# Kernel tuning notes

Hardware: AMD Instinct MI355X
Metric: run time of the kernel (lower is better)

## Reference

```python
import jax, jax.numpy as jnp
import numpy as np

# Dims: L list entries, T hutch samples, D = output_dim*inducing_size, H = 16 hidden
L, T, D, H = 32, 64, 8192, 16


def setup_inputs() -> dict:
    key = jax.random.key(0)
    k = jax.random.split(key, 4)
    return {
        "u": jax.random.normal(k[0], (L, D), jnp.float32),
        "w": jax.random.normal(k[1], (L, T, D), jnp.float32),  # Hutchinson Gaussian probes
        "W1": jax.random.normal(k[2], (H, D), jnp.float32) / np.sqrt(D).astype(np.float32),
        "b1": jnp.zeros((H,), jnp.float32),
        "W2": jax.random.normal(k[3], (D, H), jnp.float32) / np.sqrt(H).astype(np.float32),
        "b2": jnp.zeros((D,), jnp.float32),
    }


def reference(u, w, W1, b1, W2, b2):
    # f = W2 tanh(W1 u + b1) + b2 ; Jacobian J = W2 diag(1 - h^2) W1
    h = jnp.tanh(u @ W1.T + b1)                 # [L, H]
    f = h @ W2.T + b2                           # [L, D]  (f_u_list stacked)
    s = 1.0 - h * h                             # tanh' at preactivation, [L, H]
    # u_grad = J^T w  computed without materializing J: W1^T diag(s) W2^T w
    v = jnp.einsum('ltd,dh->lth', w, W2)        # W2^T w, [L, T, H]
    v = v * s[:, None, :]                       # diag(s) applied
    g = jnp.einsum('lth,hd->ltd', v, W1)        # J^T w, [L, T, D]
    traces = jnp.sum(g * w, axis=-1)            # w^T J w, [L, T]
    # mean over hutch samples, then mean over list entries -> [1, 1] like torch.mm output
    trace_final_mean = jnp.mean(traces).reshape(1, 1)
    return f, trace_final_mean
```

## Files before the change

### kernel.cpp

```cpp
#include <hip/hip_runtime.h>

typedef __attribute__((ext_vector_type(8))) short bf16x8;
typedef __attribute__((ext_vector_type(4))) float f32x4;

namespace {
constexpr int L = 32, T = 64, D = 8192, H = 16;
constexpr int M = L * T;
constexpr int KP = 32;
constexpr int CHUNK = D / KP;

constexpr size_t WS_WH  = 0;
constexpr size_t WS_WL  = WS_WH + 32 * 8192 / 2;
constexpr size_t WS_PRE = WS_WL + 32 * 8192 / 2;
constexpr size_t WS_AC  = WS_PRE + 32 * 8 * 16;
}

__device__ inline void split1(float f, short& h, short& l) {
  unsigned b = __float_as_uint(f);
  h = (short)(b >> 16);
  float lf = f - __uint_as_float(b & 0xFFFF0000u);
  l = (short)(__float_as_uint(lf) >> 16);
}

__device__ inline void split8(float4 a0, float4 a1, bf16x8& h, bf16x8& l) {
  float f[8] = {a0.x, a0.y, a0.z, a0.w, a1.x, a1.y, a1.z, a1.w};
#pragma unroll
  for (int i = 0; i < 8; ++i) {
    short hh, ll;
    split1(f[i], hh, ll);
    h[i] = hh; l[i] = ll;
  }
}

__global__ __launch_bounds__(256) void k_setup(
    const float* __restrict__ u, const float* __restrict__ W1,
    const float* __restrict__ W2,
    ushort* __restrict__ wh, ushort* __restrict__ wl,
    float* __restrict__ pre, float* __restrict__ ac,
    float* __restrict__ out) {
  int b = blockIdx.x, tid = threadIdx.x;
  if (b == 0 && tid == 0) out[(size_t)L * D] = 0.f;
  if (b < 32) {
    int d = b * 256 + tid;
    const float4* src = reinterpret_cast<const float4*>(W2 + (size_t)d * 16);
    float4 q0 = src[0], q1 = src[1], q2 = src[2], q3 = src[3];
    float v[16] = {q0.x, q0.y, q0.z, q0.w, q1.x, q1.y, q1.z, q1.w,
                   q2.x, q2.y, q2.z, q2.w, q3.x, q3.y, q3.z, q3.w};
#pragma unroll
    for (int c = 0; c < 16; ++c) {
      short hh, ll;
      split1(v[c], hh, ll);
      wh[(size_t)c * D + d] = (ushort)hh;
      wl[(size_t)c * D + d] = (ushort)ll;
    }
  } else if (b < 64) {
    int q = (b - 32) * 256 + tid;
#pragma unroll
    for (int j = 0; j < 4; ++j) {
      int idx = (q + j * 8192) * 4;
      float4 qv = *reinterpret_cast<const float4*>(W1 + idx);
      short h0, l0, h1, l1, h2, l2, h3, l3;
      split1(qv.x, h0, l0); split1(qv.y, h1, l1);
      split1(qv.z, h2, l2); split1(qv.w, h3, l3);
      ushort4 vh = {(ushort)h0, (ushort)h1, (ushort)h2, (ushort)h3};
      ushort4 vl = {(ushort)l0, (ushort)l1, (ushort)l2, (ushort)l3};
      *reinterpret_cast<ushort4*>(wh + (size_t)16 * D + idx) = vh;
      *reinterpret_cast<ushort4*>(wl + (size_t)16 * D + idx) = vl;
    }
  } else if (b < 80) {
    int t = (b - 64) * 256 + tid;
    float4 z = {0.f, 0.f, 0.f, 0.f};
    float4* dst = reinterpret_cast<float4*>(ac);
#pragma unroll
    for (int j = 0; j < 4; ++j) dst[t + j * 4096] = z;
  } else {
    int bb = b - 80;
    int kc = bb & 7, l = bb >> 3;
    int d = kc * 1024 + tid * 4;
    float4 uv = *reinterpret_cast<const float4*>(u + (size_t)l * D + d);
    float acc[16];
#pragma unroll
    for (int h = 0; h < 16; ++h) {
      float4 wv = *reinterpret_cast<const float4*>(W1 + (size_t)h * D + d);
      float t = fmaf(uv.x, wv.x, 0.f);
      t = fmaf(uv.y, wv.y, t);
      t = fmaf(uv.z, wv.z, t);
      acc[h] = fmaf(uv.w, wv.w, t);
    }
#pragma unroll
    for (int h = 0; h < 16; ++h)
      for (int off = 1; off < 64; off <<= 1) acc[h] += __shfl_xor(acc[h], off);
    __shared__ float red[4][16];
    int lane = tid & 63, wv_ = tid >> 6;
    if (lane == 0) {
#pragma unroll
      for (int h = 0; h < 16; ++h) red[wv_][h] = acc[h];
    }
    __syncthreads();
    if (tid < 16)
      pre[((size_t)l * 8 + kc) * 16 + tid] =
          red[0][tid] + red[1][tid] + red[2][tid] + red[3][tid];
  }
}

__global__ __launch_bounds__(256) void k_trace_ac(
    const float* __restrict__ w,
    const ushort* __restrict__ wh, const ushort* __restrict__ wl,
    float* __restrict__ ac) {
  int tid = threadIdx.x;
  int wave = tid >> 6, lane = tid & 63;
  int lrow = lane & 15, kg = lane >> 4;
  int kp = blockIdx.x;
  int rt = blockIdx.y * 4 + wave;
  int m0 = rt * 16;
  int k0 = kp * CHUNK;

  const float*  wrow = w  + (size_t)(m0 + lrow) * D + k0 + kg * 8;
  const ushort* bh0  = wh + (size_t)lrow * D + k0 + kg * 8;
  const ushort* bl0  = wl + (size_t)lrow * D + k0 + kg * 8;
  const ushort* bh1  = bh0 + (size_t)16 * D;
  const ushort* bl1  = bl0 + (size_t)16 * D;

  f32x4 acc0 = {0.f, 0.f, 0.f, 0.f};
  f32x4 acc1 = {0.f, 0.f, 0.f, 0.f};

#pragma unroll
  for (int kk = 0; kk < CHUNK / 32; ++kk) {
    int off = kk * 32;
    float4 a0 = *reinterpret_cast<const float4*>(wrow + off);
    float4 a1 = *reinterpret_cast<const float4*>(wrow + off + 4);
    bf16x8 ah, al;
    split8(a0, a1, ah, al);
    bf16x8 vbh0 = *reinterpret_cast<const bf16x8*>(bh0 + off);
    bf16x8 vbl0 = *reinterpret_cast<const bf16x8*>(bl0 + off);
    bf16x8 vbh1 = *reinterpret_cast<const bf16x8*>(bh1 + off);
    bf16x8 vbl1 = *reinterpret_cast<const bf16x8*>(bl1 + off);
    acc0 = __builtin_amdgcn_mfma_f32_16x16x32_bf16(ah, vbh0, acc0, 0, 0, 0);
    acc0 = __builtin_amdgcn_mfma_f32_16x16x32_bf16(ah, vbl0, acc0, 0, 0, 0);
    acc0 = __builtin_amdgcn_mfma_f32_16x16x32_bf16(al, vbh0, acc0, 0, 0, 0);
    acc1 = __builtin_amdgcn_mfma_f32_16x16x32_bf16(ah, vbh1, acc1, 0, 0, 0);
    acc1 = __builtin_amdgcn_mfma_f32_16x16x32_bf16(ah, vbl1, acc1, 0, 0, 0);
    acc1 = __builtin_amdgcn_mfma_f32_16x16x32_bf16(al, vbh1, acc1, 0, 0, 0);
  }

  float* dst = ac + (size_t)(m0 + kg * 4) * 32;
#pragma unroll
  for (int j = 0; j < 4; ++j) {
    atomicAdd(dst + (size_t)j * 32 + lrow,      acc0[j]);
    atomicAdd(dst + (size_t)j * 32 + 16 + lrow, acc1[j]);
  }
}

__global__ __launch_bounds__(256) void k_tail(
    const float* __restrict__ pre, const float* __restrict__ b1,
    const float* __restrict__ W2, const float* __restrict__ b2,
    const float* __restrict__ ac, float* __restrict__ out) {
  int b = blockIdx.x, tid = threadIdx.x;
  if (b >= 128) {
    __shared__ float s[16];
    int l = b - 128;
    if (tid < 16) {
      float p = b1[tid];
#pragma unroll
      for (int kc = 0; kc < 8; ++kc) p += pre[((size_t)l * 8 + kc) * 16 + tid];
      float t = tanhf(p);
      s[tid] = 1.f - t * t;
    }
    __syncthreads();
    if (tid < 64) {
      int m = l * 64 + tid;
      const float4* src = reinterpret_cast<const float4*>(ac + (size_t)m * 32);
      float av[16], cv[16];
#pragma unroll
      for (int j = 0; j < 4; ++j) {
        float4 q = src[j];
        av[j * 4 + 0] = q.x; av[j * 4 + 1] = q.y;
        av[j * 4 + 2] = q.z; av[j * 4 + 3] = q.w;
      }
#pragma unroll
      for (int j = 0; j < 4; ++j) {
        float4 q = src[4 + j];
        cv[j * 4 + 0] = q.x; cv[j * 4 + 1] = q.y;
        cv[j * 4 + 2] = q.z; cv[j * 4 + 3] = q.w;
      }
      float tr = 0.f;
#pragma unroll
      for (int h = 0; h < 16; ++h) tr = fmaf(s[h] * av[h], cv[h], tr);
      for (int off = 1; off < 64; off <<= 1) tr += __shfl_xor(tr, off);
      if (tid == 0) atomicAdd(out + (size_t)L * D, tr * (1.0f / (float)(L * T)));
    }
    return;
  }
  __shared__ float hl[8][16];
  int lg = b >> 5;
  if (tid < 128) {
    int ll = tid >> 4, h = tid & 15, l = lg * 8 + ll;
    float p = b1[h];
#pragma unroll
    for (int kc = 0; kc < 8; ++kc) p += pre[((size_t)l * 8 + kc) * 16 + h];
    hl[ll][h] = tanhf(p);
  }
  __syncthreads();
  int d = (b & 31) * 256 + tid;
  const float4* w2r = reinterpret_cast<const float4*>(W2 + (size_t)d * 16);
  float4 q0 = w2r[0], q1 = w2r[1], q2 = w2r[2], q3 = w2r[3];
  float w2v[16] = {q0.x, q0.y, q0.z, q0.w, q1.x, q1.y, q1.z, q1.w,
                   q2.x, q2.y, q2.z, q2.w, q3.x, q3.y, q3.z, q3.w};
  float bv = b2[d];
#pragma unroll
  for (int ll = 0; ll < 8; ++ll) {
    float fv = bv;
#pragma unroll
    for (int h = 0; h < 16; ++h) fv = fmaf(hl[ll][h], w2v[h], fv);
    out[(size_t)(lg * 8 + ll) * D + d] = fv;
  }
}

extern "C" void kernel_launch(void* const* d_in, const int* in_sizes, int n_in,
                              void* d_out, int out_size, void* d_ws, size_t ws_size,
                              hipStream_t stream) {
  const float* u  = (const float*)d_in[0];
  const float* w  = (const float*)d_in[1];
  const float* W1 = (const float*)d_in[2];
  const float* b1 = (const float*)d_in[3];
  const float* W2 = (const float*)d_in[4];
  const float* b2 = (const float*)d_in[5];
  float* out = (float*)d_out;
  float* ws  = (float*)d_ws;
  ushort* wcat_h = (ushort*)(ws + WS_WH);
  ushort* wcat_l = (ushort*)(ws + WS_WL);
  float* pre = ws + WS_PRE;
  float* acb = ws + WS_AC;

  hipLaunchKernelGGL(k_setup,    dim3(336), dim3(256), 0, stream,
                     u, W1, W2, wcat_h, wcat_l, pre, acb, out);
  hipLaunchKernelGGL(k_trace_ac, dim3(KP, 32), dim3(256), 0, stream,
                     w, wcat_h, wcat_l, acb);
  hipLaunchKernelGGL(k_tail,     dim3(160), dim3(256), 0, stream,
                     pre, b1, W2, b2, acb, out);
}
```

Baseline: 123.5 us.

## Replace atomic split-K accumulation with per-partition partials reduced in tail

```diff
diff --git a/kernel.cpp b/kernel.cpp
--- a/kernel.cpp
+++ b/kernel.cpp
@@ -6,7 +6,7 @@
 namespace {
 constexpr int L = 32, T = 64, D = 8192, H = 16;
 constexpr int M = L * T;
-constexpr int KP = 32;
+constexpr int KP = 64;
 constexpr int CHUNK = D / KP;
 
 constexpr size_t WS_WH  = 0;
@@ -36,8 +36,7 @@
     const float* __restrict__ u, const float* __restrict__ W1,
     const float* __restrict__ W2,
     ushort* __restrict__ wh, ushort* __restrict__ wl,
-    float* __restrict__ pre, float* __restrict__ ac,
-    float* __restrict__ out) {
+    float* __restrict__ pre, float* __restrict__ out) {
   int b = blockIdx.x, tid = threadIdx.x;
   if (b == 0 && tid == 0) out[(size_t)L * D] = 0.f;
   if (b < 32) {
@@ -67,14 +66,8 @@
       *reinterpret_cast<ushort4*>(wh + (size_t)16 * D + idx) = vh;
       *reinterpret_cast<ushort4*>(wl + (size_t)16 * D + idx) = vl;
     }
-  } else if (b < 80) {
-    int t = (b - 64) * 256 + tid;
-    float4 z = {0.f, 0.f, 0.f, 0.f};
-    float4* dst = reinterpret_cast<float4*>(ac);
-#pragma unroll
-    for (int j = 0; j < 4; ++j) dst[t + j * 4096] = z;
   } else {
-    int bb = b - 80;
+    int bb = b - 64;
     int kc = bb & 7, l = bb >> 3;
     int d = kc * 1024 + tid * 4;
     float4 uv = *reinterpret_cast<const float4*>(u + (size_t)l * D + d);
@@ -143,11 +136,11 @@
     acc1 = __builtin_amdgcn_mfma_f32_16x16x32_bf16(al, vbh1, acc1, 0, 0, 0);
   }
 
-  float* dst = ac + (size_t)(m0 + kg * 4) * 32;
+  float* dst = ac + ((size_t)kp * M + m0 + kg * 4) * 32;
 #pragma unroll
   for (int j = 0; j < 4; ++j) {
-    atomicAdd(dst + (size_t)j * 32 + lrow,      acc0[j]);
-    atomicAdd(dst + (size_t)j * 32 + 16 + lrow, acc1[j]);
+    dst[(size_t)j * 32 + lrow]      = acc0[j];
+    dst[(size_t)j * 32 + 16 + lrow] = acc1[j];
   }
 }
 
@@ -155,10 +148,13 @@
     const float* __restrict__ pre, const float* __restrict__ b1,
     const float* __restrict__ W2, const float* __restrict__ b2,
     const float* __restrict__ ac, float* __restrict__ out) {
+  __shared__ float hl[8][16];
+  __shared__ float s[16];
+  __shared__ float red[4];
   int b = blockIdx.x, tid = threadIdx.x;
   if (b >= 128) {
-    __shared__ float s[16];
-    int l = b - 128;
+    int bb = b - 128;
+    int l = bb >> 3;
     if (tid < 16) {
       float p = b1[tid];
 #pragma unroll
@@ -167,31 +163,24 @@
       s[tid] = 1.f - t * t;
     }
     __syncthreads();
-    if (tid < 64) {
-      int m = l * 64 + tid;
-      const float4* src = reinterpret_cast<const float4*>(ac + (size_t)m * 32);
-      float av[16], cv[16];
-#pragma unroll
-      for (int j = 0; j < 4; ++j) {
-        float4 q = src[j];
-        av[j * 4 + 0] = q.x; av[j * 4 + 1] = q.y;
-        av[j * 4 + 2] = q.z; av[j * 4 + 3] = q.w;
-      }
-#pragma unroll
-      for (int j = 0; j < 4; ++j) {
-        float4 q = src[4 + j];
-        cv[j * 4 + 0] = q.x; cv[j * 4 + 1] = q.y;
-        cv[j * 4 + 2] = q.z; cv[j * 4 + 3] = q.w;
-      }
-      float tr = 0.f;
-#pragma unroll
-      for (int h = 0; h < 16; ++h) tr = fmaf(s[h] * av[h], cv[h], tr);
-      for (int off = 1; off < 64; off <<= 1) tr += __shfl_xor(tr, off);
-      if (tid == 0) atomicAdd(out + (size_t)L * D, tr * (1.0f / (float)(L * T)));
-    }
+    int r = tid >> 5, c = tid & 31;
+    size_t m = (size_t)bb * 8 + r;
+    float acc = 0.f;
+#pragma unroll 8
+    for (int kp = 0; kp < KP; ++kp)
+      acc += ac[((size_t)kp * M + m) * 32 + c];
+    float partner = __shfl_xor(acc, 16);
+    float t = (c < 16) ? s[c] * acc * partner : 0.f;
+#pragma unroll
+    for (int off = 1; off < 64; off <<= 1) t += __shfl_xor(t, off);
+    int lane = tid & 63, wv_ = tid >> 6;
+    if (lane == 0) red[wv_] = t;
+    __syncthreads();
+    if (tid == 0)
+      atomicAdd(out + (size_t)L * D,
+                (red[0] + red[1] + red[2] + red[3]) * (1.0f / (float)(L * T)));
     return;
   }
-  __shared__ float hl[8][16];
   int lg = b >> 5;
   if (tid < 128) {
     int ll = tid >> 4, h = tid & 15, l = lg * 8 + ll;
@@ -232,10 +221,10 @@
   float* pre = ws + WS_PRE;
   float* acb = ws + WS_AC;
 
-  hipLaunchKernelGGL(k_setup,    dim3(336), dim3(256), 0, stream,
-                     u, W1, W2, wcat_h, wcat_l, pre, acb, out);
+  hipLaunchKernelGGL(k_setup,    dim3(320), dim3(256), 0, stream,
+                     u, W1, W2, wcat_h, wcat_l, pre, out);
   hipLaunchKernelGGL(k_trace_ac, dim3(KP, 32), dim3(256), 0, stream,
                      w, wcat_h, wcat_l, acb);
-  hipLaunchKernelGGL(k_tail,     dim3(160), dim3(256), 0, stream,
+  hipLaunchKernelGGL(k_tail,     dim3(384), dim3(256), 0, stream,
                      pre, b1, W2, b2, acb, out);
 }
```

Result: slower. 132.6 us (+7.3%).
